# Kernel optimization log

Hardware: AMD Instinct MI355X
Metric: run time of the kernel (lower is better)

Reference implementation:

```python
import jax, jax.numpy as jnp
import numpy as np

B, N, M, D = 4, 2048, 2048, 512
BLUR, SCALING, P = 0.05, 0.9, 2          # geomloss: blur=epsilon, p=2
DIAMETER = 2.0                            # max distance between unit-norm points
# geomloss epsilon_schedule: diameter^p annealed down to blur^p by scaling^p
_sched = np.arange(P * np.log(DIAMETER), P * np.log(BLUR), P * np.log(SCALING))
EPS_LIST = np.concatenate([[DIAMETER ** P], np.exp(_sched), [BLUR ** P]]).astype(np.float32)


def setup_inputs() -> dict:
    key = jax.random.key(0)
    k1, k2 = jax.random.split(key)
    return {
        "E_p": jax.random.normal(k1, (B, N, D), jnp.float32),
        "E_t": jax.random.normal(k2, (B, M, D), jnp.float32),
    }


def _l2norm(x):
    return x / jnp.maximum(jnp.linalg.norm(x, axis=-1, keepdims=True), 1e-12)


def _cost(x, y):
    # C(x,y) = ||x - y||^2 / 2  (geomloss squared_distances / 2 for p=2)
    x2 = jnp.sum(x * x, axis=-1)[:, :, None]   # (B, N, 1)
    y2 = jnp.sum(y * y, axis=-1)[:, None, :]   # (B, 1, M)
    return 0.5 * (x2 + y2 - 2.0 * jnp.einsum("bnd,bmd->bnm", x, y))


def _softmin(eps, C, h):
    # h: (B, M) = log_weights + potential/eps ;  returns (B, N)
    return -eps * jax.nn.logsumexp(h[:, None, :] - C / eps, axis=-1)


def _sinkhorn_divergence(x, y):
    b, n = x.shape[0], x.shape[1]
    m = y.shape[1]
    C_xy = _cost(x, y)
    C_yx = jnp.swapaxes(C_xy, 1, 2)
    C_xx = _cost(x, x)
    C_yy = _cost(y, y)
    log_a = jnp.full((b, n), -np.log(n), x.dtype)   # uniform weights
    log_b = jnp.full((b, m), -np.log(m), x.dtype)

    sg = jax.lax.stop_gradient
    Cxy_s, Cyx_s, Cxx_s, Cyy_s = sg(C_xy), sg(C_yx), sg(C_xx), sg(C_yy)

    # init at the largest epsilon (geomloss sinkhorn_loop init)
    eps0 = float(EPS_LIST[0])
    f_ba = _softmin(eps0, Cxy_s, log_b)
    g_ab = _softmin(eps0, Cyx_s, log_a)
    f_aa = _softmin(eps0, Cxx_s, log_a)
    g_bb = _softmin(eps0, Cyy_s, log_b)

    def body(carry, eps):
        f_aa, g_bb, g_ab, f_ba = carry
        ft_ba = _softmin(eps, Cxy_s, log_b + g_ab / eps)
        gt_ab = _softmin(eps, Cyx_s, log_a + f_ba / eps)
        ft_aa = _softmin(eps, Cxx_s, log_a + f_aa / eps)
        gt_bb = _softmin(eps, Cyy_s, log_b + g_bb / eps)
        new = (0.5 * (f_aa + ft_aa), 0.5 * (g_bb + gt_bb),
               0.5 * (g_ab + gt_ab), 0.5 * (f_ba + ft_ba))
        return new, None

    (f_aa, g_bb, g_ab, f_ba), _ = jax.lax.scan(
        body, (f_aa, g_bb, g_ab, f_ba), jnp.asarray(EPS_LIST))

    # last extrapolation at final eps (gradients flow through the cost only,
    # matching geomloss's detached-potential final step)
    eps = float(EPS_LIST[-1])
    f_ba_f = _softmin(eps, C_xy, sg(log_b + g_ab / eps))
    g_ab_f = _softmin(eps, C_yx, sg(log_a + f_ba / eps))
    f_aa_f = _softmin(eps, C_xx, sg(log_a + f_aa / eps))
    g_bb_f = _softmin(eps, C_yy, sg(log_b + g_bb / eps))

    a_w = jnp.exp(log_a)
    b_w = jnp.exp(log_b)
    loss = (jnp.sum(a_w * (f_ba_f - f_aa_f), axis=-1)
            + jnp.sum(b_w * (g_ab_f - g_bb_f), axis=-1))   # (B,)
    return jnp.mean(loss)


def reference(E_p, E_t):
    return _sinkhorn_divergence(_l2norm(E_p), _l2norm(E_t))
```

## Files before the change

### kernel.cpp

```cpp
#include <hip/hip_runtime.h>
#include <hip/hip_bf16.h>
#include <hip/hip_fp16.h>
#include <math.h>

#define B_ 4
#define N_ 2048
#define D_ 512

typedef __bf16    bf16x8  __attribute__((ext_vector_type(8)));
typedef float     floatx4 __attribute__((ext_vector_type(4)));
typedef _Float16  half8   __attribute__((ext_vector_type(8)));

#if __has_builtin(__builtin_amdgcn_exp2f)
__device__ __forceinline__ float fexp2(float x) { return __builtin_amdgcn_exp2f(x); }
#else
__device__ __forceinline__ float fexp2(float x) { return exp2f(x); }
#endif
#if __has_builtin(__builtin_amdgcn_logf)
__device__ __forceinline__ float flog2(float x) { return __builtin_amdgcn_logf(x); }
#else
__device__ __forceinline__ float flog2(float x) { return __log2f(x); }
#endif

__device__ __forceinline__ void gload16(const void* g, void* l) {
  __builtin_amdgcn_global_load_lds(
      (const __attribute__((address_space(1))) void*)g,
      (__attribute__((address_space(3))) void*)l, 16, 0, 0);
}

__global__ __launch_bounds__(256) void norm_kernel(const float* __restrict__ in,
                                                   __hip_bfloat16* __restrict__ out) {
  const size_t row = blockIdx.x;
  const int t = threadIdx.x;
  const float* src = in + row * D_;
  float v0 = src[t], v1 = src[t + 256];
  float ss = fmaf(v0, v0, v1 * v1);
#pragma unroll
  for (int off = 1; off < 64; off <<= 1) ss += __shfl_xor(ss, off);
  __shared__ float red[4];
  if ((t & 63) == 0) red[t >> 6] = ss;
  __syncthreads();
  const float tot = red[0] + red[1] + red[2] + red[3];
  const float scale = 1.0f / fmaxf(sqrtf(tot), 1e-12f);
  out[row * D_ + t]       = __float2bfloat16(v0 * scale);
  out[row * D_ + t + 256] = __float2bfloat16(v1 * scale);
}

__global__ __launch_bounds__(256) void gram_gemm(const __hip_bfloat16* __restrict__ X,
                                                 const __hip_bfloat16* __restrict__ Y,
                                                 __half* __restrict__ Gxy,
                                                 __half* __restrict__ Gxx,
                                                 __half* __restrict__ Gyy) {
  __shared__ __hip_bfloat16 As[128 * 32];
  __shared__ __hip_bfloat16 Bs[128 * 32];
  const int t = threadIdx.x;
  const int wave = t >> 6, lane = t & 63;
  const int bm0 = blockIdx.x * 128, bn0 = blockIdx.y * 128;
  const int mat = blockIdx.z >> 2;
  const size_t bb = blockIdx.z & 3;
  const __hip_bfloat16* Ab = (mat == 2 ? Y : X) + bb * (size_t)(N_ * D_);
  const __hip_bfloat16* Bb = (mat == 1 ? X : Y) + bb * (size_t)(N_ * D_);
  __half* Gb = (mat == 0 ? Gxy : mat == 1 ? Gxx : Gyy) + bb * (size_t)N_ * N_;

  floatx4 acc[4][4] = {};
  const int wr = wave >> 1, wc = wave & 1;
  const int srow = t >> 2;
  const int scol = (t & 3) * 8;
  char* AsB = (char*)As;
  char* BsB = (char*)Bs;
  const int ldsOff = wave * 1024;

  for (int k0 = 0; k0 < D_; k0 += 32) {
    __syncthreads();
    gload16(Ab + (size_t)(bm0 + srow)      * D_ + k0 + scol, AsB + ldsOff);
    gload16(Ab + (size_t)(bm0 + 64 + srow) * D_ + k0 + scol, AsB + 4096 + ldsOff);
    gload16(Bb + (size_t)(bn0 + srow)      * D_ + k0 + scol, BsB + ldsOff);
    gload16(Bb + (size_t)(bn0 + 64 + srow) * D_ + k0 + scol, BsB + 4096 + ldsOff);
    __syncthreads();

    const int lrow = lane & 15, lk = (lane >> 4) * 8;
    bf16x8 af[4], bfr[4];
#pragma unroll
    for (int mi = 0; mi < 4; ++mi)
      af[mi] = *(const bf16x8*)((const char*)As + ((wr * 64 + mi * 16 + lrow) * 32 + lk) * 2);
#pragma unroll
    for (int ni = 0; ni < 4; ++ni)
      bfr[ni] = *(const bf16x8*)((const char*)Bs + ((wc * 64 + ni * 16 + lrow) * 32 + lk) * 2);
#pragma unroll
    for (int mi = 0; mi < 4; ++mi)
#pragma unroll
      for (int ni = 0; ni < 4; ++ni)
        acc[mi][ni] = __builtin_amdgcn_mfma_f32_16x16x32_bf16(af[mi], bfr[ni], acc[mi][ni], 0, 0, 0);
  }

  const int orow = (lane >> 4) * 4, ocol = lane & 15;
#pragma unroll
  for (int mi = 0; mi < 4; ++mi)
#pragma unroll
    for (int ni = 0; ni < 4; ++ni) {
      const int row = bm0 + wr * 64 + mi * 16 + orow;
      const int col = bn0 + wc * 64 + ni * 16 + ocol;
#pragma unroll
      for (int r = 0; r < 4; ++r)
        Gb[(size_t)(row + r) * N_ + col] = __float2half(acc[mi][ni][r]);
    }
}

#define L2E_ 1.44269504088896f
#define LN2_ 0.69314718055995f

template <int MODE>
__global__ __launch_bounds__(256) void sink_stream(
    const __half* __restrict__ Gxy, const __half* __restrict__ Gxx,
    const __half* __restrict__ Gyy,
    const float* __restrict__ potOld, float* __restrict__ potNew,
    float* __restrict__ colPart, float eps, float* __restrict__ out) {
  __shared__ float part[4][16];

  const int bid = blockIdx.x;
  const int mat = bid % 3;
  const int rem = bid / 3;
  const int b = rem >> 7, stripe = rem & 127;
  const int lane = threadIdx.x & 63, wave = threadIdx.x >> 6;
  const int c0 = wave * 512 + lane * 8;

  const float inv_eps = 1.0f / eps;
  const float ieL  = inv_eps * L2E_;
  const float hbL  = (-7.62461898616f - inv_eps) * L2E_;
  const float negEpsLn2 = -eps * LN2_;

  const __half* G = (mat == 0 ? Gxy : mat == 1 ? Gxx : Gyy) + (size_t)b * N_ * N_;
  const int hIdx = (mat == 0) ? 1 : (mat == 1) ? 2 : 3;
  const int oIdx = (mat == 0) ? 0 : hIdx;
  const float* potH = potOld + ((size_t)hIdx * B_ + b) * N_;
  const float* potO = potOld + ((size_t)oIdx * B_ + b) * N_;
  float*       potW = potNew + ((size_t)oIdx * B_ + b) * N_;

  const int rbase = stripe * 16;

  float hh[8];
  if constexpr (MODE == 0) {
#pragma unroll
    for (int e = 0; e < 8; ++e) hh[e] = hbL;
  } else {
    const float4 a = *(const float4*)(potH + c0);
    const float4 c = *(const float4*)(potH + c0 + 4);
    hh[0] = fmaf(a.x, ieL, hbL); hh[1] = fmaf(a.y, ieL, hbL);
    hh[2] = fmaf(a.z, ieL, hbL); hh[3] = fmaf(a.w, ieL, hbL);
    hh[4] = fmaf(c.x, ieL, hbL); hh[5] = fmaf(c.y, ieL, hbL);
    hh[6] = fmaf(c.z, ieL, hbL); hh[7] = fmaf(c.w, ieL, hbL);
  }

  float hrP = hbL;
  if constexpr (MODE != 0) hrP = fmaf(potO[rbase + (lane & 15)], ieL, hbL);

  float rsum[16];
#pragma unroll
  for (int r = 0; r < 16; ++r) rsum[r] = 0.0f;
  float colsum[8];
#pragma unroll
  for (int e = 0; e < 8; ++e) colsum[e] = 0.0f;

  const __half* gbase = G + (size_t)rbase * N_ + c0;

  half8 cur[4], nxt[4];
#pragma unroll
  for (int r = 0; r < 4; ++r) cur[r] = *(const half8*)(gbase + (size_t)r * N_);

#pragma unroll
  for (int it = 0; it < 4; ++it) {
    if (it < 3) {
#pragma unroll
      for (int r = 0; r < 4; ++r)
        nxt[r] = *(const half8*)(gbase + (size_t)((it + 1) * 4 + r) * N_);
    }

#pragma unroll
    for (int r = 0; r < 4; ++r) {
      const int row = it * 4 + r;
      const float hb = __shfl(hrP, row) - hbL;
      float w[8];
#pragma unroll
      for (int e = 0; e < 8; ++e)
        w[e] = fexp2(fmaf((float)cur[r][e], ieL, hh[e] + hb));
      if (mat == 0) {
#pragma unroll
        for (int e = 0; e < 8; ++e) colsum[e] += w[e];
      }
      rsum[row] = ((w[0] + w[1]) + (w[2] + w[3])) + ((w[4] + w[5]) + (w[6] + w[7]));
    }

    if (it < 3) {
#pragma unroll
      for (int r = 0; r < 4; ++r) cur[r] = nxt[r];
    }
  }

  if (mat == 0) {
    float4 o0, o1;
    o0.x = flog2(colsum[0]) - (hh[0] - hbL);
    o0.y = flog2(colsum[1]) - (hh[1] - hbL);
    o0.z = flog2(colsum[2]) - (hh[2] - hbL);
    o0.w = flog2(colsum[3]) - (hh[3] - hbL);
    o1.x = flog2(colsum[4]) - (hh[4] - hbL);
    o1.y = flog2(colsum[5]) - (hh[5] - hbL);
    o1.z = flog2(colsum[6]) - (hh[6] - hbL);
    o1.w = flog2(colsum[7]) - (hh[7] - hbL);
    float* cp = colPart + ((size_t)(b * 128 + stripe) * 2048 + c0);
    *(float4*)cp = o0;
    *(float4*)(cp + 4) = o1;
  }

#pragma unroll
  for (int r = 0; r < 16; ++r) {
    float s = rsum[r];
#pragma unroll
    for (int off = 1; off < 64; off <<= 1) s += __shfl_xor(s, off);
    if (lane == 0) part[wave][r] = s;
  }
  __syncthreads();

  float vfin = 0.0f;
  if (wave == 0 && lane < 16) {
    const float S = part[0][lane] + part[1][lane] + part[2][lane] + part[3][lane];
    const float v = negEpsLn2 * (flog2(S) + hbL - hrP);
    const int r = rbase + lane;
    if constexpr (MODE == 0) {
      potW[r] = v;
    } else if constexpr (MODE == 1) {
      const float vOld = -negEpsLn2 * (hrP - hbL);
      potW[r] = 0.5f * (vOld + v);
    } else {
      vfin = v;
    }
  }

  if constexpr (MODE == 2) {
#pragma unroll
    for (int off = 1; off < 64; off <<= 1) vfin += __shfl_xor(vfin, off);
    if (threadIdx.x == 0) {
      const float sign = (mat == 0) ? 1.0f : -1.0f;
      atomicAdd(out, sign * vfin * (1.0f / (2048.0f * B_)));
    }
  }
}

template <int MODE>
__global__ __launch_bounds__(256) void sink_merge(
    const float* __restrict__ colPart, const float* __restrict__ potOld,
    float* __restrict__ potNew, float eps, float* __restrict__ out) {
  __shared__ float2 mp[3][64];
  const int lane = threadIdx.x & 63, sub = threadIdx.x >> 6;
  const int colg = blockIdx.x * 64 + lane;
  const int b = colg >> 11, col = colg & 2047;
  const float negEpsLn2 = -eps * LN2_;

  float m = -3.0e38f, s = 0.0f;
  const float* cp = colPart + ((size_t)(b * 128 + sub * 32)) * 2048 + col;
#pragma unroll
  for (int st = 0; st < 32; ++st) {
    const float L = cp[(size_t)st * 2048];
    const float nm = fmaxf(m, L);
    s = fmaf(s, fexp2(m - nm), fexp2(L - nm));
    m = nm;
  }
  if (sub != 0) mp[sub - 1][lane] = make_float2(m, s);
  __syncthreads();

  float vfin = 0.0f;
  if (sub == 0) {
#pragma unroll
    for (int w = 0; w < 3; ++w) {
      const float2 q = mp[w][lane];
      const float nm = fmaxf(m, q.x);
      s = fmaf(s, fexp2(m - nm), q.y * fexp2(q.x - nm));
      m = nm;
    }
    const float v = negEpsLn2 * (m + flog2(s));
    if constexpr (MODE == 0) {
      potNew[((size_t)1 * B_ + b) * N_ + col] = v;
    } else if constexpr (MODE == 1) {
      potNew[((size_t)1 * B_ + b) * N_ + col] =
          0.5f * (potOld[((size_t)1 * B_ + b) * N_ + col] + v);
    } else {
      vfin = v;
    }
  }

  if constexpr (MODE == 2) {
#pragma unroll
    for (int off = 1; off < 64; off <<= 1) vfin += __shfl_xor(vfin, off);
    __shared__ float red[4];
    if ((threadIdx.x & 63) == 0) red[sub] = vfin;
    __syncthreads();
    if (threadIdx.x == 0)
      atomicAdd(out, (red[0] + red[1] + red[2] + red[3]) * (1.0f / (2048.0f * B_)));
  }
}

extern "C" void kernel_launch(void* const* d_in, const int* in_sizes, int n_in,
                              void* d_out, int out_size, void* d_ws, size_t ws_size,
                              hipStream_t stream) {
  const float* E_p = (const float*)d_in[0];
  const float* E_t = (const float*)d_in[1];
  float* out = (float*)d_out;
  char* ws = (char*)d_ws;

  size_t off = 0;
  auto alloc = [&](size_t bytes) {
    void* p = ws + off;
    off += (bytes + 255) & ~(size_t)255;
    return p;
  };
  __hip_bfloat16* Xb = (__hip_bfloat16*)alloc((size_t)B_ * N_ * D_ * 2);
  __hip_bfloat16* Yb = (__hip_bfloat16*)alloc((size_t)B_ * N_ * D_ * 2);
  __half* Gxy = (__half*)alloc((size_t)B_ * N_ * N_ * 2);
  __half* Gxx = (__half*)alloc((size_t)B_ * N_ * N_ * 2);
  __half* Gyy = (__half*)alloc((size_t)B_ * N_ * N_ * 2);
  float* potA = (float*)alloc((size_t)4 * B_ * N_ * 4);
  float* potB = (float*)alloc((size_t)4 * B_ * N_ * 4);
  float* colPart = (float*)alloc((size_t)B_ * 128 * 2048 * 4);

  norm_kernel<<<B_ * N_, 256, 0, stream>>>(E_p, Xb);
  norm_kernel<<<B_ * N_, 256, 0, stream>>>(E_t, Yb);

  dim3 gg(16, 16, 12);
  gram_gemm<<<gg, 256, 0, stream>>>(Xb, Yb, Gxy, Gxx, Gyy);

  float epsl[48];
  int ne = 0;
  epsl[ne++] = 4.0f;
  {
    const double lstart = 2.0 * log(2.0);
    const double lstop  = 2.0 * log(0.05);
    const double lstep  = 2.0 * log(0.9);
    for (int k = 0;; ++k) {
      const double v = lstart + k * lstep;
      if (!(v > lstop)) break;
      epsl[ne++] = (float)exp(v);
    }
  }
  epsl[ne++] = 0.0025f;

  (void)hipMemsetAsync(d_out, 0, sizeof(float), stream);

  sink_stream<0><<<1536, 256, 0, stream>>>(Gxy, Gxx, Gyy, potA, potA, colPart,
                                           epsl[0], nullptr);
  sink_merge<0><<<128, 256, 0, stream>>>(colPart, potA, potA, epsl[0], nullptr);

  float* cur = potA;
  float* nxt = potB;
  for (int i = 0; i < ne; ++i) {
    sink_stream<1><<<1536, 256, 0, stream>>>(Gxy, Gxx, Gyy, cur, nxt, colPart,
                                             epsl[i], nullptr);
    sink_merge<1><<<128, 256, 0, stream>>>(colPart, cur, nxt, epsl[i], nullptr);
    float* tmp = cur; cur = nxt; nxt = tmp;
  }

  sink_stream<2><<<1536, 256, 0, stream>>>(Gxy, Gxx, Gyy, cur, cur, colPart,
                                           epsl[ne - 1], out);
  sink_merge<2><<<128, 256, 0, stream>>>(colPart, cur, cur, epsl[ne - 1], out);
}
```

Baseline: 1.318 ms.

## Give each wave full-width rows and reduce column sums in shared memory

The streaming Sinkhorn kernel is restructured so each block covers 32 rows, with each wave owning 8 full rows across all 2048 columns. Previously each wave held a 512-column slice of 16 rows. Row sums now finish with a single wave-level shuffle reduction, with no cross-wave shared-memory step. Column partials are combined across waves in a 32 KB shared buffer, which halves the number of column partial stripes. Column partials are also emitted as plain sums with a known shift (the max-free bias hbL), so the merge kernel drops its online log-sum-exp and just adds and takes one log. This costs more registers (32 column accumulators plus 32 h values), larger LDS use, half as many blocks, and it relies on the fixed bias keeping exp values in range.

```diff
diff --git a/kernel.cpp b/kernel.cpp
--- a/kernel.cpp
+++ b/kernel.cpp
@@ -115,14 +115,14 @@
     const __half* __restrict__ Gyy,
     const float* __restrict__ potOld, float* __restrict__ potNew,
     float* __restrict__ colPart, float eps, float* __restrict__ out) {
-  __shared__ float part[4][16];
+  __shared__ float cw[4][2048];
+  __shared__ float redls[4];
 
   const int bid = blockIdx.x;
   const int mat = bid % 3;
   const int rem = bid / 3;
-  const int b = rem >> 7, stripe = rem & 127;
+  const int b = rem >> 6, stripe = rem & 63;
   const int lane = threadIdx.x & 63, wave = threadIdx.x >> 6;
-  const int c0 = wave * 512 + lane * 8;
 
   const float inv_eps = 1.0f / eps;
   const float ieL  = inv_eps * L2E_;
@@ -136,111 +136,124 @@
   const float* potO = potOld + ((size_t)oIdx * B_ + b) * N_;
   float*       potW = potNew + ((size_t)oIdx * B_ + b) * N_;
 
-  const int rbase = stripe * 16;
-
-  float hh[8];
+  const int rbase = stripe * 32 + wave * 8;
+
+  float hh[32];
   if constexpr (MODE == 0) {
 #pragma unroll
-    for (int e = 0; e < 8; ++e) hh[e] = hbL;
+    for (int c = 0; c < 32; ++c) hh[c] = hbL;
   } else {
-    const float4 a = *(const float4*)(potH + c0);
-    const float4 c = *(const float4*)(potH + c0 + 4);
-    hh[0] = fmaf(a.x, ieL, hbL); hh[1] = fmaf(a.y, ieL, hbL);
-    hh[2] = fmaf(a.z, ieL, hbL); hh[3] = fmaf(a.w, ieL, hbL);
-    hh[4] = fmaf(c.x, ieL, hbL); hh[5] = fmaf(c.y, ieL, hbL);
-    hh[6] = fmaf(c.z, ieL, hbL); hh[7] = fmaf(c.w, ieL, hbL);
-  }
-
-  float hrP = hbL;
-  if constexpr (MODE != 0) hrP = fmaf(potO[rbase + (lane & 15)], ieL, hbL);
-
-  float rsum[16];
-#pragma unroll
-  for (int r = 0; r < 16; ++r) rsum[r] = 0.0f;
-  float colsum[8];
-#pragma unroll
-  for (int e = 0; e < 8; ++e) colsum[e] = 0.0f;
-
-  const __half* gbase = G + (size_t)rbase * N_ + c0;
-
-  half8 cur[4], nxt[4];
-#pragma unroll
-  for (int r = 0; r < 4; ++r) cur[r] = *(const half8*)(gbase + (size_t)r * N_);
+#pragma unroll
+    for (int p = 0; p < 4; ++p) {
+      const float4 a = *(const float4*)(potH + p * 512 + lane * 8);
+      const float4 c4 = *(const float4*)(potH + p * 512 + lane * 8 + 4);
+      hh[p * 8 + 0] = fmaf(a.x, ieL, hbL);  hh[p * 8 + 1] = fmaf(a.y, ieL, hbL);
+      hh[p * 8 + 2] = fmaf(a.z, ieL, hbL);  hh[p * 8 + 3] = fmaf(a.w, ieL, hbL);
+      hh[p * 8 + 4] = fmaf(c4.x, ieL, hbL); hh[p * 8 + 5] = fmaf(c4.y, ieL, hbL);
+      hh[p * 8 + 6] = fmaf(c4.z, ieL, hbL); hh[p * 8 + 7] = fmaf(c4.w, ieL, hbL);
+    }
+  }
+
+  float hrD[8];
+  if constexpr (MODE == 0) {
+#pragma unroll
+    for (int r = 0; r < 8; ++r) hrD[r] = 0.0f;
+  } else {
+#pragma unroll
+    for (int r = 0; r < 8; ++r) hrD[r] = potO[rbase + r] * ieL;
+  }
+
+  float colsum[32];
+#pragma unroll
+  for (int c = 0; c < 32; ++c) colsum[c] = 0.0f;
+  float rsum[8];
+
+  const __half* grow = G + (size_t)rbase * N_ + lane * 8;
 
 #pragma unroll
   for (int it = 0; it < 4; ++it) {
-    if (it < 3) {
-#pragma unroll
-      for (int r = 0; r < 4; ++r)
-        nxt[r] = *(const half8*)(gbase + (size_t)((it + 1) * 4 + r) * N_);
-    }
-
-#pragma unroll
-    for (int r = 0; r < 4; ++r) {
-      const int row = it * 4 + r;
-      const float hb = __shfl(hrP, row) - hbL;
-      float w[8];
-#pragma unroll
-      for (int e = 0; e < 8; ++e)
-        w[e] = fexp2(fmaf((float)cur[r][e], ieL, hh[e] + hb));
-      if (mat == 0) {
-#pragma unroll
-        for (int e = 0; e < 8; ++e) colsum[e] += w[e];
+    half8 r0c[4], r1c[4];
+#pragma unroll
+    for (int p = 0; p < 4; ++p) {
+      r0c[p] = *(const half8*)(grow + (size_t)(it * 2)     * N_ + p * 512);
+      r1c[p] = *(const half8*)(grow + (size_t)(it * 2 + 1) * N_ + p * 512);
+    }
+    const float h0 = hrD[it * 2], h1 = hrD[it * 2 + 1];
+    float a0 = 0.0f, a1 = 0.0f;
+#pragma unroll
+    for (int p = 0; p < 4; ++p) {
+      float s0 = 0.0f, s1 = 0.0f;
+#pragma unroll
+      for (int e = 0; e < 8; ++e) {
+        const int c = p * 8 + e;
+        const float w0 = fexp2(fmaf((float)r0c[p][e], ieL, hh[c] + h0));
+        const float w1 = fexp2(fmaf((float)r1c[p][e], ieL, hh[c] + h1));
+        s0 += w0;
+        s1 += w1;
+        if (mat == 0) colsum[c] += w0 + w1;
       }
-      rsum[row] = ((w[0] + w[1]) + (w[2] + w[3])) + ((w[4] + w[5]) + (w[6] + w[7]));
-    }
-
-    if (it < 3) {
-#pragma unroll
-      for (int r = 0; r < 4; ++r) cur[r] = nxt[r];
+      a0 += s0;
+      a1 += s1;
+    }
+    rsum[it * 2] = a0;
+    rsum[it * 2 + 1] = a1;
+  }
+
+#pragma unroll
+  for (int r = 0; r < 8; ++r) {
+    float s = rsum[r];
+#pragma unroll
+    for (int off = 1; off < 64; off <<= 1) s += __shfl_xor(s, off);
+    rsum[r] = s;
+  }
+
+  float lsum = 0.0f;
+  if (lane == 0) {
+#pragma unroll
+    for (int r = 0; r < 8; ++r) {
+      const float v = negEpsLn2 * (flog2(rsum[r]) - hrD[r]);
+      if constexpr (MODE == 0) {
+        potW[rbase + r] = v;
+      } else if constexpr (MODE == 1) {
+        const float vOld = -negEpsLn2 * hrD[r];
+        potW[rbase + r] = 0.5f * (vOld + v);
+      } else {
+        lsum += v;
+      }
     }
   }
 
   if (mat == 0) {
-    float4 o0, o1;
-    o0.x = flog2(colsum[0]) - (hh[0] - hbL);
-    o0.y = flog2(colsum[1]) - (hh[1] - hbL);
-    o0.z = flog2(colsum[2]) - (hh[2] - hbL);
-    o0.w = flog2(colsum[3]) - (hh[3] - hbL);
-    o1.x = flog2(colsum[4]) - (hh[4] - hbL);
-    o1.y = flog2(colsum[5]) - (hh[5] - hbL);
-    o1.z = flog2(colsum[6]) - (hh[6] - hbL);
-    o1.w = flog2(colsum[7]) - (hh[7] - hbL);
-    float* cp = colPart + ((size_t)(b * 128 + stripe) * 2048 + c0);
-    *(float4*)cp = o0;
-    *(float4*)(cp + 4) = o1;
-  }
-
-#pragma unroll
-  for (int r = 0; r < 16; ++r) {
-    float s = rsum[r];
-#pragma unroll
-    for (int off = 1; off < 64; off <<= 1) s += __shfl_xor(s, off);
-    if (lane == 0) part[wave][r] = s;
+#pragma unroll
+    for (int p = 0; p < 4; ++p) {
+      *(float4*)&cw[wave][p * 512 + lane * 8] =
+          make_float4(colsum[p * 8 + 0], colsum[p * 8 + 1],
+                      colsum[p * 8 + 2], colsum[p * 8 + 3]);
+      *(float4*)&cw[wave][p * 512 + lane * 8 + 4] =
+          make_float4(colsum[p * 8 + 4], colsum[p * 8 + 5],
+                      colsum[p * 8 + 6], colsum[p * 8 + 7]);
+    }
   }
   __syncthreads();
-
-  float vfin = 0.0f;
-  if (wave == 0 && lane < 16) {
-    const float S = part[0][lane] + part[1][lane] + part[2][lane] + part[3][lane];
-    const float v = negEpsLn2 * (flog2(S) + hbL - hrP);
-    const int r = rbase + lane;
-    if constexpr (MODE == 0) {
-      potW[r] = v;
-    } else if constexpr (MODE == 1) {
-      const float vOld = -negEpsLn2 * (hrP - hbL);
-      potW[r] = 0.5f * (vOld + v);
-    } else {
-      vfin = v;
-    }
+  if (mat == 0) {
+    const int cbase = threadIdx.x * 8;
+    float o[8];
+#pragma unroll
+    for (int k = 0; k < 8; ++k)
+      o[k] = ((cw[0][cbase + k] + cw[1][cbase + k]) +
+              (cw[2][cbase + k] + cw[3][cbase + k]));
+    float* cp = colPart + ((size_t)(b * 64 + stripe) * 2048 + cbase);
+    *(float4*)cp       = make_float4(o[0], o[1], o[2], o[3]);
+    *(float4*)(cp + 4) = make_float4(o[4], o[5], o[6], o[7]);
   }
 
   if constexpr (MODE == 2) {
-#pragma unroll
-    for (int off = 1; off < 64; off <<= 1) vfin += __shfl_xor(vfin, off);
+    if (lane == 0) redls[wave] = lsum;
+    __syncthreads();
     if (threadIdx.x == 0) {
       const float sign = (mat == 0) ? 1.0f : -1.0f;
-      atomicAdd(out, sign * vfin * (1.0f / (2048.0f * B_)));
+      atomicAdd(out, sign * (redls[0] + redls[1] + redls[2] + redls[3]) *
+                         (1.0f / (2048.0f * B_)));
     }
   }
 }
@@ -249,39 +262,31 @@
 __global__ __launch_bounds__(256) void sink_merge(
     const float* __restrict__ colPart, const float* __restrict__ potOld,
     float* __restrict__ potNew, float eps, float* __restrict__ out) {
-  __shared__ float2 mp[3][64];
+  __shared__ float mp[3][64];
   const int lane = threadIdx.x & 63, sub = threadIdx.x >> 6;
   const int colg = blockIdx.x * 64 + lane;
   const int b = colg >> 11, col = colg & 2047;
+  const float ieL = (1.0f / eps) * L2E_;
   const float negEpsLn2 = -eps * LN2_;
 
-  float m = -3.0e38f, s = 0.0f;
-  const float* cp = colPart + ((size_t)(b * 128 + sub * 32)) * 2048 + col;
-#pragma unroll
-  for (int st = 0; st < 32; ++st) {
-    const float L = cp[(size_t)st * 2048];
-    const float nm = fmaxf(m, L);
-    s = fmaf(s, fexp2(m - nm), fexp2(L - nm));
-    m = nm;
-  }
-  if (sub != 0) mp[sub - 1][lane] = make_float2(m, s);
+  float s = 0.0f;
+  const float* cp = colPart + ((size_t)(b * 64 + sub * 16)) * 2048 + col;
+#pragma unroll
+  for (int st = 0; st < 16; ++st) s += cp[(size_t)st * 2048];
+  if (sub != 0) mp[sub - 1][lane] = s;
   __syncthreads();
 
   float vfin = 0.0f;
   if (sub == 0) {
-#pragma unroll
-    for (int w = 0; w < 3; ++w) {
-      const float2 q = mp[w][lane];
-      const float nm = fmaxf(m, q.x);
-      s = fmaf(s, fexp2(m - nm), q.y * fexp2(q.x - nm));
-      m = nm;
-    }
-    const float v = negEpsLn2 * (m + flog2(s));
+    s += (mp[0][lane] + mp[1][lane]) + mp[2][lane];
+    const float gsh = (MODE == 0) ? 0.0f
+                    : potOld[((size_t)1 * B_ + b) * N_ + col] * ieL;
+    const float v = negEpsLn2 * (flog2(s) - gsh);
     if constexpr (MODE == 0) {
       potNew[((size_t)1 * B_ + b) * N_ + col] = v;
     } else if constexpr (MODE == 1) {
-      potNew[((size_t)1 * B_ + b) * N_ + col] =
-          0.5f * (potOld[((size_t)1 * B_ + b) * N_ + col] + v);
+      const float vOld = -negEpsLn2 * gsh;
+      potNew[((size_t)1 * B_ + b) * N_ + col] = 0.5f * (vOld + v);
     } else {
       vfin = v;
     }
@@ -319,7 +324,7 @@
   __half* Gyy = (__half*)alloc((size_t)B_ * N_ * N_ * 2);
   float* potA = (float*)alloc((size_t)4 * B_ * N_ * 4);
   float* potB = (float*)alloc((size_t)4 * B_ * N_ * 4);
-  float* colPart = (float*)alloc((size_t)B_ * 128 * 2048 * 4);
+  float* colPart = (float*)alloc((size_t)B_ * 64 * 2048 * 4);
 
   norm_kernel<<<B_ * N_, 256, 0, stream>>>(E_p, Xb);
   norm_kernel<<<B_ * N_, 256, 0, stream>>>(E_t, Yb);
@@ -344,20 +349,20 @@
 
   (void)hipMemsetAsync(d_out, 0, sizeof(float), stream);
 
-  sink_stream<0><<<1536, 256, 0, stream>>>(Gxy, Gxx, Gyy, potA, potA, colPart,
-                                           epsl[0], nullptr);
+  sink_stream<0><<<768, 256, 0, stream>>>(Gxy, Gxx, Gyy, potA, potA, colPart,
+                                          epsl[0], nullptr);
   sink_merge<0><<<128, 256, 0, stream>>>(colPart, potA, potA, epsl[0], nullptr);
 
   float* cur = potA;
   float* nxt = potB;
   for (int i = 0; i < ne; ++i) {
-    sink_stream<1><<<1536, 256, 0, stream>>>(Gxy, Gxx, Gyy, cur, nxt, colPart,
-                                             epsl[i], nullptr);
+    sink_stream<1><<<768, 256, 0, stream>>>(Gxy, Gxx, Gyy, cur, nxt, colPart,
+                                            epsl[i], nullptr);
     sink_merge<1><<<128, 256, 0, stream>>>(colPart, cur, nxt, epsl[i], nullptr);
     float* tmp = cur; cur = nxt; nxt = tmp;
   }
 
-  sink_stream<2><<<1536, 256, 0, stream>>>(Gxy, Gxx, Gyy, cur, cur, colPart,
-                                           epsl[ne - 1], out);
+  sink_stream<2><<<768, 256, 0, stream>>>(Gxy, Gxx, Gyy, cur, cur, colPart,
+                                          epsl[ne - 1], out);
   sink_merge<2><<<128, 256, 0, stream>>>(colPart, cur, cur, epsl[ne - 1], out);
 }
```

Result: slower. 1.410 ms (+7.0%).
